# Optimization experiments

Hardware: AMD Instinct MI355X
Metric: run time of the kernel (lower is better)

## Reference

```python
import jax, jax.numpy as jnp
import numpy as np

N = 50000
E = 640000
IN_DIM = 23
HID = 128
NUM_CLASS = 12


def setup_inputs() -> dict:
    key = jax.random.key(0)
    ks = jax.random.split(key, 12)
    x = jax.random.normal(ks[0], (N, IN_DIM), dtype=jnp.float32)
    edge_index = jax.random.randint(ks[1], (2, E), 0, N, dtype=jnp.int32)

    def glorot(k, shape):
        fan_in, fan_out = shape
        lim = np.sqrt(6.0 / (fan_in + fan_out)).astype(np.float32)
        return jax.random.uniform(k, shape, jnp.float32, -lim, lim)

    W1 = glorot(ks[2], (IN_DIM, HID)); b1 = jnp.zeros((HID,), jnp.float32)
    W2 = glorot(ks[3], (HID, HID));    b2 = jnp.zeros((HID,), jnp.float32)
    W3 = glorot(ks[4], (HID, HID));    b3 = jnp.zeros((HID,), jnp.float32)
    Wc1 = glorot(ks[5], (HID, 64));    bc1 = jnp.zeros((64,), jnp.float32)
    Wc2 = glorot(ks[6], (64, NUM_CLASS)); bc2 = jnp.zeros((NUM_CLASS,), jnp.float32)
    return {"x": x, "edge_index": edge_index,
            "W1": W1, "b1": b1, "W2": W2, "b2": b2, "W3": W3, "b3": b3,
            "Wc1": Wc1, "bc1": bc1, "Wc2": Wc2, "bc2": bc2}


def _gcn_norm(edge_index, n_nodes):
    # add self loops, compute symmetric normalization D^-1/2 (A+I) D^-1/2
    loop = jnp.arange(n_nodes, dtype=edge_index.dtype)
    src = jnp.concatenate([edge_index[0], loop])
    dst = jnp.concatenate([edge_index[1], loop])
    deg = jax.ops.segment_sum(jnp.ones_like(dst, dtype=jnp.float32), dst,
                              num_segments=n_nodes)
    dinv = jax.lax.rsqrt(deg)  # deg >= 1 due to self loops
    norm = dinv[src] * dinv[dst]  # [E + N]
    return src, dst, norm


def _gcn_layer(h, W, b, src, dst, norm, n_nodes):
    h = h @ W                          # linear (bias applied after aggregation, per PyG)
    msg = h[src] * norm[:, None]       # gather + scale
    out = jax.ops.segment_sum(msg, dst, num_segments=n_nodes)  # scatter-add
    return out + b


def reference(x, edge_index, W1, b1, W2, b2, W3, b3, Wc1, bc1, Wc2, bc2):
    n = x.shape[0]
    src, dst, norm = _gcn_norm(edge_index, n)
    h = jnp.tanh(_gcn_layer(x, W1, b1, src, dst, norm, n))
    h = jnp.tanh(_gcn_layer(h, W2, b2, src, dst, norm, n))
    h = jnp.tanh(_gcn_layer(h, W3, b3, src, dst, norm, n))
    # dropout is identity in eval mode
    out = h @ Wc1 + bc1
    out = out @ Wc2 + bc2
    return out
```

## Files before the change

kernel.cpp:

```cpp
#include <hip/hip_runtime.h>
#include <math.h>

#define NN 50000
#define EE 640000
#define IND 23
#define HID 128
#define MIDD 64
#define NCLS 12
#define NB 49
#define QS 32766.0f
#define INVQS (1.0f / 32766.0f)

typedef short short8v __attribute__((ext_vector_type(8)));


__global__ void k_count(const int* __restrict__ dst, int* __restrict__ cnt, int e) {
    int i = blockIdx.x * blockDim.x + threadIdx.x;
    if (i < e) atomicAdd(&cnt[dst[i]], 1);
}

__global__ __launch_bounds__(256) void k_scan_local(const int* __restrict__ cnt,
                                                    int* __restrict__ row_ptr,
                                                    float* __restrict__ dinv,
                                                    int* __restrict__ sums) {
    __shared__ int wtot[4];
    const int tid = threadIdx.x;
    const int wid = tid >> 6, lane = tid & 63;
    const int base = blockIdx.x * 1024 + tid * 4;
    int v[4];
#pragma unroll
    for (int t = 0; t < 4; ++t) {
        int i = base + t;
        v[t] = (i < NN) ? cnt[i] : 0;
        if (i < NN) dinv[i] = rsqrtf((float)v[t] + 1.0f);
    }
    int slocal = v[0] + v[1] + v[2] + v[3];
    int val = slocal;
#pragma unroll
    for (int off = 1; off < 64; off <<= 1) {
        int t = __shfl_up(val, off, 64);
        if (lane >= off) val += t;
    }
    if (lane == 63) wtot[wid] = val;
    __syncthreads();
    int woff = 0;
#pragma unroll
    for (int w = 0; w < 4; ++w) woff += (w < wid) ? wtot[w] : 0;
    int run = woff + val - slocal;
#pragma unroll
    for (int t = 0; t < 4; ++t) {
        int i = base + t;
        if (i < NN) row_ptr[i] = run;
        run += v[t];
    }
    if (tid == 255) sums[blockIdx.x] = woff + val;
}

__global__ void k_scan_sums(const int* __restrict__ sums, int* __restrict__ offs,
                            int* __restrict__ row_ptr) {
    const int lane = threadIdx.x;
    int v = (lane < NB) ? sums[lane] : 0;
    int val = v;
#pragma unroll
    for (int off = 1; off < 64; off <<= 1) {
        int t = __shfl_up(val, off, 64);
        if (lane >= off) val += t;
    }
    if (lane < NB) offs[lane] = val - v;
    if (lane == NB - 1) row_ptr[NN] = val;
}

__global__ __launch_bounds__(256) void k_scan_apply(int* __restrict__ row_ptr,
                                                    const int* __restrict__ offs,
                                                    int* __restrict__ cursor) {
    const int base = blockIdx.x * 1024 + threadIdx.x * 4;
    const int o = offs[blockIdx.x];
#pragma unroll
    for (int t = 0; t < 4; ++t) {
        int i = base + t;
        if (i < NN) {
            int rp = row_ptr[i] + o;
            row_ptr[i] = rp;
            cursor[i] = rp;
        }
    }
}

__global__ void k_fill(const int* __restrict__ src, const int* __restrict__ dst,
                       int* __restrict__ cursor, int* __restrict__ e_src, int e) {
    int i = blockIdx.x * blockDim.x + threadIdx.x;
    if (i < e) {
        int d = dst[i];
        int pos = atomicAdd(&cursor[d], 1);
        e_src[pos] = src[i];
    }
}

__global__ __launch_bounds__(256) void k_pad(const float* __restrict__ x,
                                             const float* __restrict__ dinv,
                                             float* __restrict__ xp) {
    int i = blockIdx.x * 256 + threadIdx.x;
    int node = i >> 5, f = i & 31;
    xp[i] = (f < IND) ? x[node * IND + f] * dinv[node] : 0.f;
}

__global__ __launch_bounds__(256) void k_l1(const float* __restrict__ xp,
                                            const float* __restrict__ W1,
                                            const float* __restrict__ b1,
                                            const int* __restrict__ row_ptr,
                                            const int* __restrict__ e_src,
                                            const float* __restrict__ dinv,
                                            short* __restrict__ outq) {
    const int tid = threadIdx.x;
    const int i = blockIdx.x * 4 + (tid >> 6);
    const int lane = tid & 63;
    const int slot = lane >> 3;
    const int f = lane & 7;
    const float4* xp4 = (const float4*)xp;
    const int beg = row_ptr[i];
    const int deg = row_ptr[i + 1] - beg;
    float4 acc = make_float4(0.f, 0.f, 0.f, 0.f);
    for (int base = 0; base < deg; base += 64) {
        const int cnt = min(64, deg - base);
        int s_l = 0;
        if (lane < cnt) s_l = e_src[beg + base + lane];
        int e = 0;
        for (; e + 8 <= cnt; e += 8) {
            int s = __shfl(s_l, e + slot, 64);
            float4 v = xp4[s * 8 + f];
            acc.x += v.x; acc.y += v.y; acc.z += v.z; acc.w += v.w;
        }
        if (e < cnt) {
            int s = __shfl(s_l, e + slot, 64);
            if (e + slot < cnt) {
                float4 v = xp4[s * 8 + f];
                acc.x += v.x; acc.y += v.y; acc.z += v.z; acc.w += v.w;
            }
        }
    }
#pragma unroll
    for (int off = 32; off >= 8; off >>= 1) {
        acc.x += __shfl_down(acc.x, off, 64);
        acc.y += __shfl_down(acc.y, off, 64);
        acc.z += __shfl_down(acc.z, off, 64);
        acc.w += __shfl_down(acc.w, off, 64);
    }
    const float di = dinv[i];
    if (lane < 8) {
        float4 v = xp4[i * 8 + lane];
        acc.x = (acc.x + v.x) * di; acc.y = (acc.y + v.y) * di;
        acc.z = (acc.z + v.z) * di; acc.w = (acc.w + v.w) * di;
    }
    float a0 = b1[lane], a1 = b1[lane + 64];
#pragma unroll
    for (int k = 0; k < IND; ++k) {
        float comp = ((k & 3) == 0) ? acc.x : ((k & 3) == 1) ? acc.y
                   : ((k & 3) == 2) ? acc.z : acc.w;
        float xk = __shfl(comp, k >> 2, 64);
        a0 += xk * W1[k * HID + lane];
        a1 += xk * W1[k * HID + lane + 64];
    }
    outq[i * HID + lane]      = (short)__float2int_rn(tanhf(a0) * QS);
    outq[i * HID + lane + 64] = (short)__float2int_rn(tanhf(a1) * QS);
}

__global__ __launch_bounds__(256) void k_aggq(const short* __restrict__ hq,
                                              const int* __restrict__ row_ptr,
                                              const int* __restrict__ e_src,
                                              const float* __restrict__ dinv,
                                              float* __restrict__ aggf) {
    const int tid = threadIdx.x;
    const int i = blockIdx.x * 4 + (tid >> 6);
    const int lane = tid & 63;
    const int slot = lane >> 4;
    const int f = lane & 15;
    const short8v* h8 = (const short8v*)hq;
    const int beg = row_ptr[i];
    const int deg = row_ptr[i + 1] - beg;
    float facc[8];
#pragma unroll
    for (int t = 0; t < 8; ++t) facc[t] = 0.f;
    for (int base = 0; base < deg; base += 64) {
        const int cnt = min(64, deg - base);
        int s_l = 0; float n_l = 0.f;
        if (lane < cnt) {
            s_l = e_src[beg + base + lane];
            n_l = dinv[s_l];
        }
        int e = 0;
#pragma unroll 2
        for (; e + 4 <= cnt; e += 4) {
            int s = __shfl(s_l, e + slot, 64);
            float nr = __shfl(n_l, e + slot, 64);
            short8v v = h8[s * 16 + f];
#pragma unroll
            for (int t = 0; t < 8; ++t) facc[t] += (float)v[t] * nr;
        }
        if (e < cnt) {
            int s = __shfl(s_l, e + slot, 64);
            float nr = __shfl(n_l, e + slot, 64);
            if (e + slot < cnt) {
                short8v v = h8[s * 16 + f];
#pragma unroll
                for (int t = 0; t < 8; ++t) facc[t] += (float)v[t] * nr;
            }
        }
    }
#pragma unroll
    for (int off = 32; off >= 16; off >>= 1)
#pragma unroll
        for (int t = 0; t < 8; ++t) facc[t] += __shfl_down(facc[t], off, 64);
    if (lane < 16) {
        const float di = dinv[i];
        const float sc = di * INVQS;
        short8v v = h8[i * 16 + lane];
        float4 o0, o1;
        o0.x = (facc[0] + di * (float)v[0]) * sc;
        o0.y = (facc[1] + di * (float)v[1]) * sc;
        o0.z = (facc[2] + di * (float)v[2]) * sc;
        o0.w = (facc[3] + di * (float)v[3]) * sc;
        o1.x = (facc[4] + di * (float)v[4]) * sc;
        o1.y = (facc[5] + di * (float)v[5]) * sc;
        o1.z = (facc[6] + di * (float)v[6]) * sc;
        o1.w = (facc[7] + di * (float)v[7]) * sc;
        ((float4*)aggf)[i * 32 + lane * 2]     = o0;
        ((float4*)aggf)[i * 32 + lane * 2 + 1] = o1;
    }
}

__global__ __launch_bounds__(256) void k_gemmT(const float* __restrict__ hin,
                                               const float* __restrict__ W,
                                               const float* __restrict__ bias,
                                               short* __restrict__ qout,
                                               float* __restrict__ fout) {
    __shared__ float Hs[64 * 36];
    __shared__ float Ws[32 * 128];
    const int tid = threadIdx.x;
    const int b0 = blockIdx.x * 64;
    const int ng = tid >> 4;
    const int cg = tid & 15;
    const float4* hin4 = (const float4*)hin;
    const float4* W4 = (const float4*)W;

    float acc[4][8];
#pragma unroll
    for (int m = 0; m < 4; ++m)
#pragma unroll
        for (int c = 0; c < 8; ++c) acc[m][c] = 0.f;

    for (int ks = 0; ks < HID; ks += 32) {
#pragma unroll
        for (int t = 0; t < 2; ++t) {
            int id = t * 256 + tid;
            int row = id >> 3;
            int k4 = id & 7;
            int node = b0 + row;
            float4 v = make_float4(0.f, 0.f, 0.f, 0.f);
            if (node < NN) v = hin4[node * 32 + (ks >> 2) + k4];
            *(float4*)&Hs[row * 36 + k4 * 4] = v;
        }
#pragma unroll
        for (int t = 0; t < 4; ++t) {
            int id = t * 256 + tid;
            int row = id >> 5;
            int c4 = id & 31;
            *(float4*)&Ws[row * 128 + c4 * 4] = W4[(ks + row) * 32 + c4];
        }
        __syncthreads();
#pragma unroll 8
        for (int kk = 0; kk < 32; ++kk) {
            float4 w0 = *(float4*)&Ws[kk * 128 + cg * 8];
            float4 w1 = *(float4*)&Ws[kk * 128 + cg * 8 + 4];
#pragma unroll
            for (int m = 0; m < 4; ++m) {
                float hv = Hs[(ng * 4 + m) * 36 + kk];
                acc[m][0] += hv * w0.x; acc[m][1] += hv * w0.y;
                acc[m][2] += hv * w0.z; acc[m][3] += hv * w0.w;
                acc[m][4] += hv * w1.x; acc[m][5] += hv * w1.y;
                acc[m][6] += hv * w1.z; acc[m][7] += hv * w1.w;
            }
        }
        __syncthreads();
    }
    const float4* b4 = (const float4*)bias;
    float4 bb0 = b4[cg * 2], bb1 = b4[cg * 2 + 1];
#pragma unroll
    for (int m = 0; m < 4; ++m) {
        int node = b0 + ng * 4 + m;
        if (node < NN) {
            float t0 = tanhf(acc[m][0] + bb0.x);
            float t1 = tanhf(acc[m][1] + bb0.y);
            float t2 = tanhf(acc[m][2] + bb0.z);
            float t3 = tanhf(acc[m][3] + bb0.w);
            float t4 = tanhf(acc[m][4] + bb1.x);
            float t5 = tanhf(acc[m][5] + bb1.y);
            float t6 = tanhf(acc[m][6] + bb1.z);
            float t7 = tanhf(acc[m][7] + bb1.w);
            if (qout) {
                short8v qv;
                qv[0] = (short)__float2int_rn(t0 * QS);
                qv[1] = (short)__float2int_rn(t1 * QS);
                qv[2] = (short)__float2int_rn(t2 * QS);
                qv[3] = (short)__float2int_rn(t3 * QS);
                qv[4] = (short)__float2int_rn(t4 * QS);
                qv[5] = (short)__float2int_rn(t5 * QS);
                qv[6] = (short)__float2int_rn(t6 * QS);
                qv[7] = (short)__float2int_rn(t7 * QS);
                ((short8v*)qout)[node * 16 + cg] = qv;
            }
            if (fout) {
                ((float4*)fout)[node * 32 + cg * 2]     = make_float4(t0, t1, t2, t3);
                ((float4*)fout)[node * 32 + cg * 2 + 1] = make_float4(t4, t5, t6, t7);
            }
        }
    }
}


__global__ __launch_bounds__(256) void k_cls(const float* __restrict__ h,
                                             const float* __restrict__ Wc1,
                                             const float* __restrict__ bc1,
                                             const float* __restrict__ Wc2,
                                             const float* __restrict__ bc2,
                                             float* __restrict__ out) {
    __shared__ float hs[16 * 128];
    __shared__ float ms[16 * 65];
    const int tid = threadIdx.x;
    const int b0 = blockIdx.x * 16;
    const float4* h4 = (const float4*)h;
#pragma unroll
    for (int t = 0; t < 2; ++t) {
        int id = t * 256 + tid;
        int node = id >> 5;
        int k4 = id & 31;
        float4 v = make_float4(0.f, 0.f, 0.f, 0.f);
        if (b0 + node < NN) v = h4[(b0 + node) * 32 + k4];
        *(float4*)&hs[node * 128 + k4 * 4] = v;
    }
    __syncthreads();
    const int q = tid >> 6;
    const int c = tid & 63;
    float acc[4];
#pragma unroll
    for (int t = 0; t < 4; ++t) acc[t] = 0.f;
    for (int k = 0; k < HID; ++k) {
        float w = Wc1[k * MIDD + c];
#pragma unroll
        for (int t = 0; t < 4; ++t) acc[t] += hs[(q + 4 * t) * 128 + k] * w;
    }
    float bb = bc1[c];
#pragma unroll
    for (int t = 0; t < 4; ++t) ms[(q + 4 * t) * 65 + c] = acc[t] + bb;
    __syncthreads();
    if (tid < 16 * NCLS) {
        int m = tid / NCLS;
        int cls = tid % NCLS;
        int node = b0 + m;
        if (node < NN) {
            float o = bc2[cls];
#pragma unroll 8
            for (int k = 0; k < MIDD; ++k) o += ms[m * 65 + k] * Wc2[k * NCLS + cls];
            out[node * NCLS + cls] = o;
        }
    }
}


extern "C" void kernel_launch(void* const* d_in, const int* in_sizes, int n_in,
                              void* d_out, int out_size, void* d_ws, size_t ws_size,
                              hipStream_t stream) {
    const float* x    = (const float*)d_in[0];
    const int*   edge = (const int*)d_in[1];
    const int*   src  = edge;
    const int*   dst  = edge + EE;
    const float* W1  = (const float*)d_in[2];  const float* b1  = (const float*)d_in[3];
    const float* W2  = (const float*)d_in[4];  const float* b2  = (const float*)d_in[5];
    const float* W3  = (const float*)d_in[6];  const float* b3  = (const float*)d_in[7];
    const float* Wc1 = (const float*)d_in[8];  const float* bc1 = (const float*)d_in[9];
    const float* Wc2 = (const float*)d_in[10]; const float* bc2 = (const float*)d_in[11];
    float* outp = (float*)d_out;

    char* p = (char*)d_ws;
    int*   cnt     = (int*)p;   p += 200064;
    int*   row_ptr = (int*)p;   p += 200064;
    float* dinv    = (float*)p; p += 200064;
    int*   sums    = (int*)p;   p += 256;
    int*   offs    = (int*)p;   p += 256;
    int*   e_src   = (int*)p;   p += (size_t)EE * 4;
    float* xp      = (float*)p; p += (size_t)NN * 32 * 4;
    short* q       = (short*)p; p += (size_t)NN * HID * 2;
    float* aggf    = (float*)p; p += (size_t)NN * HID * 4;

    hipMemsetAsync(cnt, 0, (size_t)NN * 4, stream);
    k_count     <<<(EE + 255) / 256, 256, 0, stream>>>(dst, cnt, EE);
    k_scan_local<<<NB, 256, 0, stream>>>(cnt, row_ptr, dinv, sums);
    k_scan_sums <<<1, 64, 0, stream>>>(sums, offs, row_ptr);
    k_scan_apply<<<NB, 256, 0, stream>>>(row_ptr, offs, cnt);
    k_fill      <<<(EE + 255) / 256, 256, 0, stream>>>(src, dst, cnt, e_src, EE);
    k_pad       <<<(NN * 32) / 256, 256, 0, stream>>>(x, dinv, xp);

    k_l1  <<<NN / 4, 256, 0, stream>>>(xp, W1, b1, row_ptr, e_src, dinv, q);
    k_aggq <<<NN / 4, 256, 0, stream>>>(q, row_ptr, e_src, dinv, aggf);
    k_gemmT<<<(NN + 63) / 64, 256, 0, stream>>>(aggf, W2, b2, q, nullptr);
    k_aggq <<<NN / 4, 256, 0, stream>>>(q, row_ptr, e_src, dinv, aggf);
    k_gemmT<<<(NN + 63) / 64, 256, 0, stream>>>(aggf, W3, b3, nullptr, aggf);
    k_cls<<<(NN + 15) / 16, 256, 0, stream>>>(aggf, Wc1, bc1, Wc2, bc2, outp);
}
```

Measured before the change: 341.6 us.

## Fuse classifier into last GEMM, precompose classifier weights, pack edge norms

Precomputes the product Wc1·Wc2 and the matching combined bias in a small kernel. The final transform kernel then applies the composed 128x12 classifier directly from shared memory, so the separate classifier kernel and the float round trip of the last hidden layer are gone. Edges are stored as (src, dinv[src]) pairs, which removes the dependent dinv gather in aggregation. The GEMM inner loop now reads float4 from shared memory, and the aggregation unroll goes from 2 to 4. Costs are a larger edge array and slight reassociation of the classifier arithmetic.

```diff
diff --git a/kernel.cpp b/kernel.cpp
--- a/kernel.cpp
+++ b/kernel.cpp
@@ -87,12 +87,15 @@
 }
 
 __global__ void k_fill(const int* __restrict__ src, const int* __restrict__ dst,
-                       int* __restrict__ cursor, int* __restrict__ e_src, int e) {
+                       int* __restrict__ cursor, const float* __restrict__ dinv,
+                       int2* __restrict__ e_sn, int e) {
     int i = blockIdx.x * blockDim.x + threadIdx.x;
     if (i < e) {
+        int s = src[i];
         int d = dst[i];
+        float w = dinv[s];
         int pos = atomicAdd(&cursor[d], 1);
-        e_src[pos] = src[i];
+        e_sn[pos] = make_int2(s, __float_as_int(w));
     }
 }
 
@@ -104,11 +107,30 @@
     xp[i] = (f < IND) ? x[node * IND + f] * dinv[node] : 0.f;
 }
 
+__global__ void k_wcc(const float* __restrict__ Wc1, const float* __restrict__ bc1,
+                      const float* __restrict__ Wc2, const float* __restrict__ bc2,
+                      float* __restrict__ Wcc, float* __restrict__ bcc) {
+    int t = blockIdx.x * 256 + threadIdx.x;
+    if (t < HID * NCLS) {
+        int k = t / NCLS, c = t % NCLS;
+        float s = 0.f;
+#pragma unroll 8
+        for (int j = 0; j < MIDD; ++j) s += Wc1[k * MIDD + j] * Wc2[j * NCLS + c];
+        Wcc[t] = s;
+    }
+    if (t < NCLS) {
+        float s = bc2[t];
+#pragma unroll 8
+        for (int j = 0; j < MIDD; ++j) s += bc1[j] * Wc2[j * NCLS + t];
+        bcc[t] = s;
+    }
+}
+
 __global__ __launch_bounds__(256) void k_l1(const float* __restrict__ xp,
                                             const float* __restrict__ W1,
                                             const float* __restrict__ b1,
                                             const int* __restrict__ row_ptr,
-                                            const int* __restrict__ e_src,
+                                            const int2* __restrict__ e_sn,
                                             const float* __restrict__ dinv,
                                             short* __restrict__ outq) {
     const int tid = threadIdx.x;
@@ -123,7 +145,7 @@
     for (int base = 0; base < deg; base += 64) {
         const int cnt = min(64, deg - base);
         int s_l = 0;
-        if (lane < cnt) s_l = e_src[beg + base + lane];
+        if (lane < cnt) s_l = e_sn[beg + base + lane].x;
         int e = 0;
         for (; e + 8 <= cnt; e += 8) {
             int s = __shfl(s_l, e + slot, 64);
@@ -166,7 +188,7 @@
 
 __global__ __launch_bounds__(256) void k_aggq(const short* __restrict__ hq,
                                               const int* __restrict__ row_ptr,
-                                              const int* __restrict__ e_src,
+                                              const int2* __restrict__ e_sn,
                                               const float* __restrict__ dinv,
                                               float* __restrict__ aggf) {
     const int tid = threadIdx.x;
@@ -184,11 +206,12 @@
         const int cnt = min(64, deg - base);
         int s_l = 0; float n_l = 0.f;
         if (lane < cnt) {
-            s_l = e_src[beg + base + lane];
-            n_l = dinv[s_l];
+            int2 sn = e_sn[beg + base + lane];
+            s_l = sn.x;
+            n_l = __int_as_float(sn.y);
         }
         int e = 0;
-#pragma unroll 2
+#pragma unroll 4
         for (; e + 4 <= cnt; e += 4) {
             int s = __shfl(s_l, e + slot, 64);
             float nr = __shfl(n_l, e + slot, 64);
@@ -232,9 +255,12 @@
                                                const float* __restrict__ W,
                                                const float* __restrict__ bias,
                                                short* __restrict__ qout,
-                                               float* __restrict__ fout) {
-    __shared__ float Hs[64 * 36];
-    __shared__ float Ws[32 * 128];
+                                               const float* __restrict__ Wcc,
+                                               const float* __restrict__ bcc,
+                                               float* __restrict__ outp) {
+    __shared__ float Smem[64 * 36 + 32 * 128];
+    float* Hs = Smem;
+    float* Ws = Smem + 64 * 36;
     const int tid = threadIdx.x;
     const int b0 = blockIdx.x * 64;
     const int ng = tid >> 4;
@@ -267,17 +293,25 @@
             *(float4*)&Ws[row * 128 + c4 * 4] = W4[(ks + row) * 32 + c4];
         }
         __syncthreads();
-#pragma unroll 8
-        for (int kk = 0; kk < 32; ++kk) {
-            float4 w0 = *(float4*)&Ws[kk * 128 + cg * 8];
-            float4 w1 = *(float4*)&Ws[kk * 128 + cg * 8 + 4];
-#pragma unroll
-            for (int m = 0; m < 4; ++m) {
-                float hv = Hs[(ng * 4 + m) * 36 + kk];
-                acc[m][0] += hv * w0.x; acc[m][1] += hv * w0.y;
-                acc[m][2] += hv * w0.z; acc[m][3] += hv * w0.w;
-                acc[m][4] += hv * w1.x; acc[m][5] += hv * w1.y;
-                acc[m][6] += hv * w1.z; acc[m][7] += hv * w1.w;
+#pragma unroll
+        for (int kk = 0; kk < 32; kk += 4) {
+            float4 h4[4];
+#pragma unroll
+            for (int m = 0; m < 4; ++m)
+                h4[m] = *(float4*)&Hs[(ng * 4 + m) * 36 + kk];
+#pragma unroll
+            for (int j = 0; j < 4; ++j) {
+                float4 w0 = *(float4*)&Ws[(kk + j) * 128 + cg * 8];
+                float4 w1 = *(float4*)&Ws[(kk + j) * 128 + cg * 8 + 4];
+#pragma unroll
+                for (int m = 0; m < 4; ++m) {
+                    float hv = (j == 0) ? h4[m].x : (j == 1) ? h4[m].y
+                             : (j == 2) ? h4[m].z : h4[m].w;
+                    acc[m][0] += hv * w0.x; acc[m][1] += hv * w0.y;
+                    acc[m][2] += hv * w0.z; acc[m][3] += hv * w0.w;
+                    acc[m][4] += hv * w1.x; acc[m][5] += hv * w1.y;
+                    acc[m][6] += hv * w1.z; acc[m][7] += hv * w1.w;
+                }
             }
         }
         __syncthreads();
@@ -286,81 +320,83 @@
     float4 bb0 = b4[cg * 2], bb1 = b4[cg * 2 + 1];
 #pragma unroll
     for (int m = 0; m < 4; ++m) {
-        int node = b0 + ng * 4 + m;
-        if (node < NN) {
-            float t0 = tanhf(acc[m][0] + bb0.x);
-            float t1 = tanhf(acc[m][1] + bb0.y);
-            float t2 = tanhf(acc[m][2] + bb0.z);
-            float t3 = tanhf(acc[m][3] + bb0.w);
-            float t4 = tanhf(acc[m][4] + bb1.x);
-            float t5 = tanhf(acc[m][5] + bb1.y);
-            float t6 = tanhf(acc[m][6] + bb1.z);
-            float t7 = tanhf(acc[m][7] + bb1.w);
-            if (qout) {
+        acc[m][0] = tanhf(acc[m][0] + bb0.x);
+        acc[m][1] = tanhf(acc[m][1] + bb0.y);
+        acc[m][2] = tanhf(acc[m][2] + bb0.z);
+        acc[m][3] = tanhf(acc[m][3] + bb0.w);
+        acc[m][4] = tanhf(acc[m][4] + bb1.x);
+        acc[m][5] = tanhf(acc[m][5] + bb1.y);
+        acc[m][6] = tanhf(acc[m][6] + bb1.z);
+        acc[m][7] = tanhf(acc[m][7] + bb1.w);
+    }
+
+    if (outp == nullptr) {
+#pragma unroll
+        for (int m = 0; m < 4; ++m) {
+            int node = b0 + ng * 4 + m;
+            if (node < NN && qout) {
                 short8v qv;
-                qv[0] = (short)__float2int_rn(t0 * QS);
-                qv[1] = (short)__float2int_rn(t1 * QS);
-                qv[2] = (short)__float2int_rn(t2 * QS);
-                qv[3] = (short)__float2int_rn(t3 * QS);
-                qv[4] = (short)__float2int_rn(t4 * QS);
-                qv[5] = (short)__float2int_rn(t5 * QS);
-                qv[6] = (short)__float2int_rn(t6 * QS);
-                qv[7] = (short)__float2int_rn(t7 * QS);
+                qv[0] = (short)__float2int_rn(acc[m][0] * QS);
+                qv[1] = (short)__float2int_rn(acc[m][1] * QS);
+                qv[2] = (short)__float2int_rn(acc[m][2] * QS);
+                qv[3] = (short)__float2int_rn(acc[m][3] * QS);
+                qv[4] = (short)__float2int_rn(acc[m][4] * QS);
+                qv[5] = (short)__float2int_rn(acc[m][5] * QS);
+                qv[6] = (short)__float2int_rn(acc[m][6] * QS);
+                qv[7] = (short)__float2int_rn(acc[m][7] * QS);
                 ((short8v*)qout)[node * 16 + cg] = qv;
             }
-            if (fout) {
-                ((float4*)fout)[node * 32 + cg * 2]     = make_float4(t0, t1, t2, t3);
-                ((float4*)fout)[node * 32 + cg * 2 + 1] = make_float4(t4, t5, t6, t7);
+        }
+        return;
+    }
+
+    float* H3 = Smem;
+    float* WccS = Smem + 32 * 132;
+    float* bccS = WccS + HID * NCLS;
+    for (int t = tid; t < HID * NCLS; t += 256) WccS[t] = Wcc[t];
+    if (tid < NCLS) bccS[tid] = bcc[tid];
+#pragma unroll
+    for (int h = 0; h < 2; ++h) {
+        if (h) __syncthreads();
+        if ((ng >> 3) == h) {
+            int r = (ng - h * 8) * 4;
+#pragma unroll
+            for (int m = 0; m < 4; ++m) {
+                *(float4*)&H3[(r + m) * 132 + cg * 8] =
+                    make_float4(acc[m][0], acc[m][1], acc[m][2], acc[m][3]);
+                *(float4*)&H3[(r + m) * 132 + cg * 8 + 4] =
+                    make_float4(acc[m][4], acc[m][5], acc[m][6], acc[m][7]);
             }
         }
-    }
-}
-
-
-__global__ __launch_bounds__(256) void k_cls(const float* __restrict__ h,
-                                             const float* __restrict__ Wc1,
-                                             const float* __restrict__ bc1,
-                                             const float* __restrict__ Wc2,
-                                             const float* __restrict__ bc2,
-                                             float* __restrict__ out) {
-    __shared__ float hs[16 * 128];
-    __shared__ float ms[16 * 65];
-    const int tid = threadIdx.x;
-    const int b0 = blockIdx.x * 16;
-    const float4* h4 = (const float4*)h;
-#pragma unroll
-    for (int t = 0; t < 2; ++t) {
-        int id = t * 256 + tid;
-        int node = id >> 5;
-        int k4 = id & 31;
-        float4 v = make_float4(0.f, 0.f, 0.f, 0.f);
-        if (b0 + node < NN) v = h4[(b0 + node) * 32 + k4];
-        *(float4*)&hs[node * 128 + k4 * 4] = v;
-    }
-    __syncthreads();
-    const int q = tid >> 6;
-    const int c = tid & 63;
-    float acc[4];
-#pragma unroll
-    for (int t = 0; t < 4; ++t) acc[t] = 0.f;
-    for (int k = 0; k < HID; ++k) {
-        float w = Wc1[k * MIDD + c];
-#pragma unroll
-        for (int t = 0; t < 4; ++t) acc[t] += hs[(q + 4 * t) * 128 + k] * w;
-    }
-    float bb = bc1[c];
-#pragma unroll
-    for (int t = 0; t < 4; ++t) ms[(q + 4 * t) * 65 + c] = acc[t] + bb;
-    __syncthreads();
-    if (tid < 16 * NCLS) {
-        int m = tid / NCLS;
-        int cls = tid % NCLS;
-        int node = b0 + m;
-        if (node < NN) {
-            float o = bc2[cls];
-#pragma unroll 8
-            for (int k = 0; k < MIDD; ++k) o += ms[m * 65 + k] * Wc2[k * NCLS + cls];
-            out[node * NCLS + cls] = o;
+        __syncthreads();
+        const int n32 = tid >> 3, oct = tid & 7;
+        float a0 = 0.f, a1 = 0.f, a2 = 0.f, a3 = 0.f, a4 = 0.f, a5 = 0.f,
+              a6 = 0.f, a7 = 0.f, a8 = 0.f, a9 = 0.f, a10 = 0.f, a11 = 0.f;
+#pragma unroll
+        for (int kk = 0; kk < 16; ++kk) {
+            int k = kk * 8 + oct;
+            float hv = H3[n32 * 132 + k];
+            const float4* wr = (const float4*)&WccS[k * NCLS];
+            float4 wa = wr[0], wb = wr[1], wc = wr[2];
+            a0 += hv * wa.x; a1 += hv * wa.y; a2  += hv * wa.z; a3  += hv * wa.w;
+            a4 += hv * wb.x; a5 += hv * wb.y; a6  += hv * wb.z; a7  += hv * wb.w;
+            a8 += hv * wc.x; a9 += hv * wc.y; a10 += hv * wc.z; a11 += hv * wc.w;
+        }
+#pragma unroll
+        for (int off = 4; off; off >>= 1) {
+            a0 += __shfl_down(a0, off, 64);   a1 += __shfl_down(a1, off, 64);
+            a2 += __shfl_down(a2, off, 64);   a3 += __shfl_down(a3, off, 64);
+            a4 += __shfl_down(a4, off, 64);   a5 += __shfl_down(a5, off, 64);
+            a6 += __shfl_down(a6, off, 64);   a7 += __shfl_down(a7, off, 64);
+            a8 += __shfl_down(a8, off, 64);   a9 += __shfl_down(a9, off, 64);
+            a10 += __shfl_down(a10, off, 64); a11 += __shfl_down(a11, off, 64);
+        }
+        int node = b0 + h * 32 + n32;
+        if (oct == 0 && node < NN) {
+            float4* op = (float4*)&outp[node * NCLS];
+            op[0] = make_float4(a0 + bccS[0], a1 + bccS[1], a2 + bccS[2], a3 + bccS[3]);
+            op[1] = make_float4(a4 + bccS[4], a5 + bccS[5], a6 + bccS[6], a7 + bccS[7]);
+            op[2] = make_float4(a8 + bccS[8], a9 + bccS[9], a10 + bccS[10], a11 + bccS[11]);
         }
     }
 }
@@ -386,23 +422,25 @@
     float* dinv    = (float*)p; p += 200064;
     int*   sums    = (int*)p;   p += 256;
     int*   offs    = (int*)p;   p += 256;
-    int*   e_src   = (int*)p;   p += (size_t)EE * 4;
+    int2*  e_sn    = (int2*)p;  p += (size_t)EE * 8;
     float* xp      = (float*)p; p += (size_t)NN * 32 * 4;
     short* q       = (short*)p; p += (size_t)NN * HID * 2;
     float* aggf    = (float*)p; p += (size_t)NN * HID * 4;
+    float* Wcc     = (float*)p; p += HID * NCLS * 4;
+    float* bcc     = (float*)p; p += 256;
 
     hipMemsetAsync(cnt, 0, (size_t)NN * 4, stream);
+    k_wcc       <<<(HID * NCLS + 255) / 256, 256, 0, stream>>>(Wc1, bc1, Wc2, bc2, Wcc, bcc);
     k_count     <<<(EE + 255) / 256, 256, 0, stream>>>(dst, cnt, EE);
     k_scan_local<<<NB, 256, 0, stream>>>(cnt, row_ptr, dinv, sums);
     k_scan_sums <<<1, 64, 0, stream>>>(sums, offs, row_ptr);
     k_scan_apply<<<NB, 256, 0, stream>>>(row_ptr, offs, cnt);
-    k_fill      <<<(EE + 255) / 256, 256, 0, stream>>>(src, dst, cnt, e_src, EE);
+    k_fill      <<<(EE + 255) / 256, 256, 0, stream>>>(src, dst, cnt, dinv, e_sn, EE);
     k_pad       <<<(NN * 32) / 256, 256, 0, stream>>>(x, dinv, xp);
 
-    k_l1  <<<NN / 4, 256, 0, stream>>>(xp, W1, b1, row_ptr, e_src, dinv, q);
-    k_aggq <<<NN / 4, 256, 0, stream>>>(q, row_ptr, e_src, dinv, aggf);
-    k_gemmT<<<(NN + 63) / 64, 256, 0, stream>>>(aggf, W2, b2, q, nullptr);
-    k_aggq <<<NN / 4, 256, 0, stream>>>(q, row_ptr, e_src, dinv, aggf);
-    k_gemmT<<<(NN + 63) / 64, 256, 0, stream>>>(aggf, W3, b3, nullptr, aggf);
-    k_cls<<<(NN + 15) / 16, 256, 0, stream>>>(aggf, Wc1, bc1, Wc2, bc2, outp);
-}
+    k_l1  <<<NN / 4, 256, 0, stream>>>(xp, W1, b1, row_ptr, e_sn, dinv, q);
+    k_aggq <<<NN / 4, 256, 0, stream>>>(q, row_ptr, e_sn, dinv, aggf);
+    k_gemmT<<<(NN + 63) / 64, 256, 0, stream>>>(aggf, W2, b2, q, nullptr, nullptr, nullptr);
+    k_aggq <<<NN / 4, 256, 0, stream>>>(q, row_ptr, e_sn, dinv, aggf);
+    k_gemmT<<<(NN + 63) / 64, 256, 0, stream>>>(aggf, W3, b3, nullptr, Wcc, bcc, outp);
+}
```

Result: faster. 331.0 us (-3.1%).
